# Kernel optimization log

Hardware: AMD Instinct MI355X
Metric: run time of the kernel (lower is better)

Reference implementation:

```python
import jax, jax.numpy as jnp
import numpy as np

B, N, INTER, RNN, W = 256, 128, 128, 128, 8


def _rms(x):
    # x / sqrt(mean(x^2, dim=2))
    return x / jnp.sqrt(jnp.mean(x * x, axis=2, keepdims=True))


def _sage(x, src, dst, deg, wl, bl, wr):
    # PyG SAGEConv(mean aggr, normalize=True): lin_l(mean_j x_j) + lin_r(x), then L2-normalize.
    # edge_index from torch.combinations(arange(k),2).t(): src=row0 (i<j), dst=row1;
    # batch repeat duplicates edges without node offsets -> mean unchanged, only nodes <N aggregate.
    agg = jax.ops.segment_sum(x[src], dst, num_segments=x.shape[0]) / deg[:, None]
    out = agg @ wl.T + bl + x @ wr.T
    nrm = jnp.maximum(jnp.linalg.norm(out, axis=-1, keepdims=True), 1e-12)
    return out / nrm


def setup_inputs() -> dict:
    key = jax.random.key(0)
    ks = jax.random.split(key, 32)
    g = lambda i, shape: jax.random.normal(ks[i], shape, dtype=jnp.float32) * 0.05
    return {
        'flows': jax.random.normal(ks[0], (B, N, N), dtype=jnp.float32),
        'coords_emb': jax.random.normal(ks[1], (B, N, 2 * N), dtype=jnp.float32),
        # Encoder_Coords: 4 pointwise Conv1d layers (kernel=1 == per-token Linear)
        'cw1': g(2, (INTER, 2 * N)), 'cb1': g(3, (INTER,)),
        'cw2': g(4, (2 * INTER, INTER)), 'cb2': g(5, (2 * INTER,)),
        'cw3': g(6, (RNN, 2 * INTER)), 'cb3': g(7, (RNN,)),
        'cw4': g(8, (RNN, RNN)), 'cb4': g(9, (RNN,)),
        # Encoder_Flows: 4 SAGEConv layers (lin_l with bias, lin_r no bias)
        'g1_wl': g(10, (INTER, N)), 'g1_bl': g(11, (INTER,)), 'g1_wr': g(12, (INTER, N)),
        'g2_wl': g(13, (2 * INTER, INTER)), 'g2_bl': g(14, (2 * INTER,)), 'g2_wr': g(15, (2 * INTER, INTER)),
        'g3_wl': g(16, (INTER, 2 * INTER)), 'g3_bl': g(17, (INTER,)), 'g3_wr': g(18, (INTER, 2 * INTER)),
        'g4_wl': g(19, (RNN, INTER)), 'g4_bl': g(20, (RNN,)), 'g4_wr': g(21, (RNN, INTER)),
        # Worker: per-worker Q/K projections (bias=False), stacked [W, out, in]
        'qca': g(22, (W, RNN, RNN)), 'kca': g(23, (W, RNN, RNN)),
        'qsa': g(24, (W, RNN, RNN)), 'ksa': g(25, (W, RNN, RNN)),
        # s_1s[0], s_2s[0]: Linear(N*W -> N, bias=False)
        's1w': g(26, (N, N * W)), 's2w': g(27, (N, N * W)),
    }


def reference(flows, coords_emb, cw1, cb1, cw2, cb2, cw3, cb3, cw4, cb4,
              g1_wl, g1_bl, g1_wr, g2_wl, g2_bl, g2_wr, g3_wl, g3_bl, g3_wr,
              g4_wl, g4_bl, g4_wr, qca, kca, qsa, ksa, s1w, s2w):
    # ---- rms_norm inputs (Model.action) ----
    f_in = _rms(flows)
    c_in = _rms(coords_emb)

    # ---- Encoder_Flows: SAGE stack over flattened [B*N, N] nodes ----
    x = f_in.reshape(-1, N)                      # [B*N, N]
    src, dst = jnp.triu_indices(N, k=1)          # combinations(arange(N), r=2)
    deg = jnp.maximum(
        jax.ops.segment_sum(jnp.ones_like(src, dtype=x.dtype), dst, num_segments=x.shape[0]), 1.0)
    x = _sage(x, src, dst, deg, g1_wl, g1_bl, g1_wr)
    x = _sage(x, src, dst, deg, g2_wl, g2_bl, g2_wr)
    x = _sage(x, src, dst, deg, g3_wl, g3_bl, g3_wr)
    x = _sage(x, src, dst, deg, g4_wl, g4_bl, g4_wr)
    f = _rms(jax.nn.relu(x).reshape(B, N, RNN))

    # ---- Encoder_Coords: 4 pointwise convs (no nonlinearity), attn=False ----
    c = c_in @ cw1.T + cb1
    c = c @ cw2.T + cb2
    c = c @ cw3.T + cb3
    c = c @ cw4.T + cb4
    c = _rms(c)

    # ---- Worker (dropout=0.0 -> identity) ----
    scale = jnp.sqrt(jnp.float32(RNN))
    # cross-attention branch (result discarded by Worker.forward, kept for fidelity)
    Qc = jnp.einsum('bnd,wod->bwno', f, qca)
    Kc = jnp.einsum('bmd,wod->bwmo', c, kca)
    ca = jnp.einsum('bwno,bwmo->bwnm', Qc, Kc) / scale
    ca = ca.transpose(0, 2, 3, 1).reshape(B, N, N * W) @ s1w.T  # [B,N,N], unused
    # self-attention branch (returned)
    Qs = jnp.einsum('bnd,wod->bwno', f, qsa)
    Ks = jnp.einsum('bmd,wod->bwmo', f, ksa)
    sa = jnp.einsum('bwno,bwmo->bwnm', Qs, Ks) / scale          # [B,W,N,N]
    sa = sa.transpose(0, 2, 3, 1).reshape(B, N, N * W) @ s2w.T  # [B,N,N]
    return sa
```

## Files before the change

### kernel.cpp

```cpp
#include <hip/hip_runtime.h>
#include <math.h>


typedef __attribute__((ext_vector_type(8))) short bf16x8;
typedef __attribute__((ext_vector_type(4))) float f32x4;

__device__ inline ushort f2b(float x) {
  unsigned u = __builtin_bit_cast(unsigned, x);
  unsigned r = (u + 0x7fffu + ((u >> 16) & 1u)) >> 16;
  return (ushort)r;
}
__device__ inline int ftswz(int e) { return ((e & 7) ^ ((e >> 3) & 15)) << 4; }
__device__ inline int cAddrRow(int rl) { return (rl < 8) ? rl * 512 : 8192 + (rl - 8) * 512; }

__device__ inline void ctr_signal(unsigned* c) {
  __threadfence();
  __syncthreads();
  if (threadIdx.x == 0)
    __hip_atomic_fetch_add(c, 1u, __ATOMIC_RELEASE, __HIP_MEMORY_SCOPE_AGENT);
}
__device__ inline void ctr_wait(unsigned* c, unsigned tgt) {
  if (threadIdx.x == 0) {
    while (__hip_atomic_load(c, __ATOMIC_ACQUIRE, __HIP_MEMORY_SCOPE_AGENT) < tgt)
      __builtin_amdgcn_s_sleep(8);
  }
  __syncthreads();
}

__global__ __launch_bounds__(256) void prep_all_k(
    const float* __restrict__ s2w,
    const float* __restrict__ wl1, const float* __restrict__ wl2,
    const float* __restrict__ wl3, const float* __restrict__ wl4,
    const float* __restrict__ wr1, const float* __restrict__ wr2,
    const float* __restrict__ wr3, const float* __restrict__ wr4,
    ushort* __restrict__ SBp, ushort* __restrict__ WL, ushort* __restrict__ WR,
    ushort* __restrict__ WRp, float* __restrict__ SS, unsigned* __restrict__ CTR) {
  if (blockIdx.x == 0) {
    SS[threadIdx.x] = 0.f;
    SS[threadIdx.x + 256] = 0.f;
    if (threadIdx.x < 8) CTR[threadIdx.x] = 0u;
  }
  int i = blockIdx.x * 256 + threadIdx.x;
  if (i < 131072) {
    int w = i >> 14, p = (i >> 7) & 127, m = i & 127;
    int sidx = ((((w * 2 + (p >> 6)) * 4 + ((p >> 4) & 3)) * 4 + (m >> 5)) * 64 +
                ((m >> 3) & 3) * 16 + (p & 15)) * 8 + (m & 7);
    SBp[sidx] = f2b(s2w[p * 1024 + m * 8 + w]);
    return;
  }
  i -= 131072;
  if (i < 98304) {
    float v, u;
    int base, K, col, k;
    if (i < 16384)      { v = wl1[i];         u = wr1[i];         base = 0;     K = 128; col = i >> 7;            k = i & 127; }
    else if (i < 49152) { int j = i - 16384;  v = wl2[j]; u = wr2[j]; base = 16384; K = 128; col = j >> 7;       k = j & 127; }
    else if (i < 81920) { int j = i - 49152;  v = wl3[j]; u = wr3[j]; base = 49152; K = 256; col = j >> 8;       k = j & 255; }
    else                { int j = i - 81920;  v = wl4[j]; u = wr4[j]; base = 81920; K = 128; col = j >> 7;       k = j & 127; }
    WL[i] = f2b(v);
    ushort ub = f2b(u);
    WR[i] = ub;
    int pidx = base + (((col >> 4) * (K / 32) + (k >> 5)) * 64 +
                       ((k >> 3) & 3) * 16 + (col & 15)) * 8 + (k & 7);
    WRp[pidx] = ub;
  }
}

template <int K, int N, int MODE>
__device__ void chain_dev(char* XS, char* C0T, float* sArr,
                          const float* __restrict__ flows, const ushort* __restrict__ XTsrc,
                          const float* __restrict__ SSprev,
                          const ushort* __restrict__ Wl, const ushort* __restrict__ Wr,
                          const float* __restrict__ bias,
                          ushort* __restrict__ XTdst, float* __restrict__ YTdst,
                          float* __restrict__ SScur, int cbid) {
  const int tid = threadIdx.x;
  const int lane = tid & 63, wv = tid >> 6, lr = lane & 15, lg = lane >> 4;
  const int cG = cbid * 16 + lr;
  constexpr int NH = K / 128;

  float sr[2][4];
  f32x4 acc1[2] = {{0.f,0.f,0.f,0.f},{0.f,0.f,0.f,0.f}};
  f32x4 acc2[2] = {{0.f,0.f,0.f,0.f},{0.f,0.f,0.f,0.f}};

  #pragma unroll
  for (int h = 0; h < NH; ++h) {
    __syncthreads();
    if (MODE == 0) {
      #pragma unroll
      for (int it = 0; it < 16; ++it) {
        int idx = tid + it * 256;
        int row = idx >> 5, c4 = idx & 31;
        const float4 v = *reinterpret_cast<const float4*>(flows + (size_t)row * 128 + c4 * 4);
        float ss = v.x * v.x + v.y * v.y + v.z * v.z + v.w * v.w;
        ss += __shfl_xor(ss, 16); ss += __shfl_xor(ss, 8);
        ss += __shfl_xor(ss, 4);  ss += __shfl_xor(ss, 2); ss += __shfl_xor(ss, 1);
        *reinterpret_cast<ushort*>(XS + (c4 * 4 + 0) * 272 + row * 2) = f2b(v.x);
        *reinterpret_cast<ushort*>(XS + (c4 * 4 + 1) * 272 + row * 2) = f2b(v.y);
        *reinterpret_cast<ushort*>(XS + (c4 * 4 + 2) * 272 + row * 2) = f2b(v.z);
        *reinterpret_cast<ushort*>(XS + (c4 * 4 + 3) * 272 + row * 2) = f2b(v.w);
        if ((tid & 31) == 0) sArr[row] = rsqrtf(ss * (1.0f / 128.0f));
      }
    } else {
      for (int e = tid * 8; e < 16384; e += 2048) {
        uint4 v = *reinterpret_cast<const uint4*>(XTsrc + h * 16384 + e);
        *reinterpret_cast<uint4*>(XS + (e >> 7) * 272 + (e & 127) * 2) = v;
      }
      if (h == 0 && tid < 128) sArr[tid] = 1.0f / fmaxf(sqrtf(SSprev[tid]), 1e-12f);
    }
    __syncthreads();

    #pragma unroll
    for (int mt = 0; mt < 2; ++mt) {
      int R = wv * 32 + mt * 16 + lr;
      bf16x8 a[4];
      #pragma unroll
      for (int ks = 0; ks < 4; ++ks) {
        union { ushort us[8]; bf16x8 v; } u;
        #pragma unroll
        for (int j = 0; j < 8; ++j)
          u.us[j] = *reinterpret_cast<const ushort*>(XS + (ks * 32 + lg * 8 + j) * 272 + R * 2);
        a[ks] = u.v;
      }
      if (h == 0) {
        #pragma unroll
        for (int rr = 0; rr < 4; ++rr) sr[mt][rr] = sArr[wv * 32 + mt * 16 + 4 * lg + rr];
      }
      #pragma unroll
      for (int ks = 0; ks < 4; ++ks) {
        bf16x8 bw = *reinterpret_cast<const bf16x8*>(Wl + (size_t)cG * K + h * 128 + ks * 32 + lg * 8);
        acc1[mt] = __builtin_amdgcn_mfma_f32_16x16x32_bf16(a[ks], bw, acc1[mt], 0, 0, 0);
      }
      #pragma unroll
      for (int ks = 0; ks < 4; ++ks) {
        bf16x8 bw = *reinterpret_cast<const bf16x8*>(Wr + (size_t)cG * K + h * 128 + ks * 32 + lg * 8);
        acc2[mt] = __builtin_amdgcn_mfma_f32_16x16x32_bf16(a[ks], bw, acc2[mt], 0, 0, 0);
      }
    }
  }

  bf16x8 aL[2][4];
  #pragma unroll
  for (int mt = 0; mt < 2; ++mt) {
    int rowL = wv * 32 + mt * 16 + lr;
    ushort iv = f2b(1.0f / (float)(rowL > 1 ? rowL : 1));
    #pragma unroll
    for (int ks = 0; ks < 4; ++ks)
      #pragma unroll
      for (int j = 0; j < 8; ++j) {
        int k = ks * 32 + lg * 8 + j;
        aL[mt][ks][j] = (short)((k < rowL) ? iv : 0);
      }
  }

  #pragma unroll
  for (int mt = 0; mt < 2; ++mt) {
    int m0 = wv * 32 + mt * 16 + lg * 4;
    uint2 pk;
    pk.x = (unsigned)f2b(acc1[mt][0] * sr[mt][0]) | ((unsigned)f2b(acc1[mt][1] * sr[mt][1]) << 16);
    pk.y = (unsigned)f2b(acc1[mt][2] * sr[mt][2]) | ((unsigned)f2b(acc1[mt][3] * sr[mt][3]) << 16);
    *reinterpret_cast<uint2*>(C0T + lr * 256 + ((2 * m0) ^ ((lr & 7) << 4))) = pk;
  }
  __syncthreads();

  {
    bf16x8 bc[4];
    #pragma unroll
    for (int ks = 0; ks < 4; ++ks)
      bc[ks] = *reinterpret_cast<const bf16x8*>(C0T + lr * 256 + ((ks * 64 + lg * 16) ^ ((lr & 7) << 4)));
    float bb = bias[cG];
    #pragma unroll
    for (int mt = 0; mt < 2; ++mt) {
      f32x4 cacc = {0.f, 0.f, 0.f, 0.f};
      #pragma unroll
      for (int ks = 0; ks < 4; ++ks)
        cacc = __builtin_amdgcn_mfma_f32_16x16x32_bf16(aL[mt][ks], bc[ks], cacc, 0, 0, 0);
      int m0 = wv * 32 + mt * 16 + lg * 4;
      float ssq[4];
      if (MODE < 2) {
        float y0 = acc2[mt][0] * sr[mt][0] + bb + cacc[0];
        float y1 = acc2[mt][1] * sr[mt][1] + bb + cacc[1];
        float y2 = acc2[mt][2] * sr[mt][2] + bb + cacc[2];
        float y3 = acc2[mt][3] * sr[mt][3] + bb + cacc[3];
        uint2 pk;
        pk.x = (unsigned)f2b(y0) | ((unsigned)f2b(y1) << 16);
        pk.y = (unsigned)f2b(y2) | ((unsigned)f2b(y3) << 16);
        *reinterpret_cast<uint2*>(&XTdst[(size_t)cG * 128 + m0]) = pk;
        ssq[0] = y0 * y0; ssq[1] = y1 * y1; ssq[2] = y2 * y2; ssq[3] = y3 * y3;
      } else {
        float4 vv;
        vv.x = fmaxf(acc2[mt][0] * sr[mt][0] + bb + cacc[0], 0.f);
        vv.y = fmaxf(acc2[mt][1] * sr[mt][1] + bb + cacc[1], 0.f);
        vv.z = fmaxf(acc2[mt][2] * sr[mt][2] + bb + cacc[2], 0.f);
        vv.w = fmaxf(acc2[mt][3] * sr[mt][3] + bb + cacc[3], 0.f);
        *reinterpret_cast<float4*>(&YTdst[(size_t)cG * 128 + m0]) = vv;
        ssq[0] = vv.x * vv.x; ssq[1] = vv.y * vv.y; ssq[2] = vv.z * vv.z; ssq[3] = vv.w * vv.w;
      }
      #pragma unroll
      for (int rr = 0; rr < 4; ++rr) {
        float ss = ssq[rr];
        ss += __shfl_xor(ss, 1); ss += __shfl_xor(ss, 2);
        ss += __shfl_xor(ss, 4); ss += __shfl_xor(ss, 8);
        if (lr == 0) atomicAdd(&SScur[m0 + rr], ss);
      }
    }
  }
}

__device__ inline void sage_stage(const float* __restrict__ flows, int blk,
                                  char* W, float* sArr, int wv, int lane) {
  int r2 = lane >> 5;
  int c4 = lane & 31;
  #pragma unroll
  for (int it = 0; it < 8; ++it) {
    int rl0 = it * 2;
    const float4 v = *reinterpret_cast<const float4*>(
        flows + ((size_t)blk * 64 + wv * 16 + rl0) * 128 + lane * 4);
    int rl = rl0 + r2;
    float ss = v.x * v.x + v.y * v.y + v.z * v.z + v.w * v.w;
    ss += __shfl_xor(ss, 16); ss += __shfl_xor(ss, 8);
    ss += __shfl_xor(ss, 4);  ss += __shfl_xor(ss, 2); ss += __shfl_xor(ss, 1);
    uint2 pk;
    pk.x = (unsigned)f2b(v.x) | ((unsigned)f2b(v.y) << 16);
    pk.y = (unsigned)f2b(v.z) | ((unsigned)f2b(v.w) << 16);
    *reinterpret_cast<uint2*>(W + rl * 256 + ((c4 * 8) ^ ((rl & 7) << 4))) = pk;
    if (c4 == 0) sArr[wv * 16 + rl] = rsqrtf(ss * (1.0f / 128.0f));
  }
}

template <int N, int DSTC>
__device__ inline void sage_l128(const char* src, char* dstW,
                                 const float* sP, float* sN,
                                 const ushort* __restrict__ Wrp,
                                 const float* __restrict__ bias,
                                 int wv, int lr, int lg, int l64) {
  bf16x8 a[4];
  float sr[4];
  #pragma unroll
  for (int ks = 0; ks < 4; ++ks)
    a[ks] = *reinterpret_cast<const bf16x8*>(src + lr * 256 + ((ks * 64 + lg * 16) ^ ((lr & 7) << 4)));
  #pragma unroll
  for (int rr = 0; rr < 4; ++rr) sr[rr] = sP[wv * 16 + 4 * lg + rr];
  float ssq[4] = {0.f, 0.f, 0.f, 0.f};
  #pragma unroll
  for (int nt = 0; nt < N / 16; ++nt) {
    int col = nt * 16 + lr;
    bf16x8 b[4];
    #pragma unroll
    for (int ks = 0; ks < 4; ++ks)
      b[ks] = *reinterpret_cast<const bf16x8*>(Wrp + (((size_t)nt * 4 + ks) * 64 + l64) * 8);
    f32x4 acc = {0.f, 0.f, 0.f, 0.f};
    #pragma unroll
    for (int ks = 0; ks < 4; ++ks)
      acc = __builtin_amdgcn_mfma_f32_16x16x32_bf16(a[ks], b[ks], acc, 0, 0, 0);
    float bb = bias[col];
    #pragma unroll
    for (int rr = 0; rr < 4; ++rr) {
      int rl = 4 * lg + rr;
      float y = acc[rr] * sr[rr] + bb;
      int rowbase = DSTC ? cAddrRow(rl) : rl * 256;
      *reinterpret_cast<ushort*>(dstW + rowbase + ((col * 2) ^ ((rl & 7) << 4))) = f2b(y);
      ssq[rr] += y * y;
    }
  }
  #pragma unroll
  for (int rr = 0; rr < 4; ++rr) {
    float ss = ssq[rr];
    ss += __shfl_xor(ss, 1); ss += __shfl_xor(ss, 2);
    ss += __shfl_xor(ss, 4); ss += __shfl_xor(ss, 8);
    if (lr == 0) sN[wv * 16 + 4 * lg + rr] = 1.0f / fmaxf(sqrtf(ss), 1e-12f);
  }
}

__device__ inline void sage_l3(const char* W, char* dstD,
                               const float* sP, float* sN,
                               const ushort* __restrict__ Wrp,
                               const float* __restrict__ bias,
                               int wv, int lr, int lg, int l64) {
  bf16x8 a[8];
  float sr[4];
  #pragma unroll
  for (int ks = 0; ks < 8; ++ks)
    a[ks] = *reinterpret_cast<const bf16x8*>(W + cAddrRow(lr) + ((ks * 64 + lg * 16) ^ ((lr & 7) << 4)));
  #pragma unroll
  for (int rr = 0; rr < 4; ++rr) sr[rr] = sP[wv * 16 + 4 * lg + rr];
  float ssq[4] = {0.f, 0.f, 0.f, 0.f};
  #pragma unroll
  for (int nt = 0; nt < 8; ++nt) {
    int col = nt * 16 + lr;
    f32x4 acc = {0.f, 0.f, 0.f, 0.f};
    #pragma unroll
    for (int ks = 0; ks < 8; ++ks) {
      bf16x8 b = *reinterpret_cast<const bf16x8*>(Wrp + (((size_t)nt * 8 + ks) * 64 + l64) * 8);
      acc = __builtin_amdgcn_mfma_f32_16x16x32_bf16(a[ks], b, acc, 0, 0, 0);
    }
    float bb = bias[col];
    #pragma unroll
    for (int rr = 0; rr < 4; ++rr) {
      int rl = 4 * lg + rr;
      float y = acc[rr] * sr[rr] + bb;
      *reinterpret_cast<ushort*>(dstD + rl * 256 + ((col * 2) ^ ((rl & 7) << 4))) = f2b(y);
      ssq[rr] += y * y;
    }
  }
  #pragma unroll
  for (int rr = 0; rr < 4; ++rr) {
    float ss = ssq[rr];
    ss += __shfl_xor(ss, 1); ss += __shfl_xor(ss, 2);
    ss += __shfl_xor(ss, 4); ss += __shfl_xor(ss, 8);
    if (lr == 0) sN[wv * 16 + 4 * lg + rr] = 1.0f / fmaxf(sqrtf(ss), 1e-12f);
  }
}

__device__ inline void sage_l4(const char* src, const float* sP,
                               const ushort* __restrict__ Wrp,
                               const float* __restrict__ bias,
                               int wv, int lr, int lg, int l64,
                               ushort* __restrict__ Fg, int blk) {
  bf16x8 a[4];
  float sr[4];
  #pragma unroll
  for (int ks = 0; ks < 4; ++ks)
    a[ks] = *reinterpret_cast<const bf16x8*>(src + lr * 256 + ((ks * 64 + lg * 16) ^ ((lr & 7) << 4)));
  #pragma unroll
  for (int rr = 0; rr < 4; ++rr) sr[rr] = sP[wv * 16 + 4 * lg + rr];
  float yreg[8][4];
  float ssq[4] = {0.f, 0.f, 0.f, 0.f};
  #pragma unroll
  for (int nt = 0; nt < 8; ++nt) {
    int col = nt * 16 + lr;
    bf16x8 b[4];
    #pragma unroll
    for (int ks = 0; ks < 4; ++ks)
      b[ks] = *reinterpret_cast<const bf16x8*>(Wrp + (((size_t)nt * 4 + ks) * 64 + l64) * 8);
    f32x4 acc = {0.f, 0.f, 0.f, 0.f};
    #pragma unroll
    for (int ks = 0; ks < 4; ++ks)
      acc = __builtin_amdgcn_mfma_f32_16x16x32_bf16(a[ks], b[ks], acc, 0, 0, 0);
    float bb = bias[col];
    #pragma unroll
    for (int rr = 0; rr < 4; ++rr) {
      float y = acc[rr] * sr[rr] + bb;
      yreg[nt][rr] = y;
      float v = fmaxf(y, 0.f);
      ssq[rr] += v * v;
    }
  }
  float sc[4];
  #pragma unroll
  for (int rr = 0; rr < 4; ++rr) {
    float ss = ssq[rr];
    ss += __shfl_xor(ss, 1); ss += __shfl_xor(ss, 2);
    ss += __shfl_xor(ss, 4); ss += __shfl_xor(ss, 8);
    sc[rr] = sqrtf(128.0f / fmaxf(ss, 1e-20f));
  }
  #pragma unroll
  for (int nt = 0; nt < 8; ++nt)
    #pragma unroll
    for (int rr = 0; rr < 4; ++rr) {
      int row = wv * 16 + 4 * lg + rr;
      Fg[((size_t)blk * 64 + row) * 128 + nt * 16 + lr] = f2b(fmaxf(yreg[nt][rr], 0.f) * sc[rr]);
    }
}

__global__ __launch_bounds__(256, 2) void mega3_k(
    const float* __restrict__ flows,
    const float* __restrict__ qsa, const float* __restrict__ ksa,
    const ushort* __restrict__ WL, const ushort* __restrict__ WR,
    const ushort* __restrict__ WRp,
    const float* __restrict__ bl1, const float* __restrict__ bl2,
    const float* __restrict__ bl3, const float* __restrict__ bl4,
    ushort* __restrict__ Fg, ushort* __restrict__ MBT,
    ushort* __restrict__ XT1, ushort* __restrict__ XT2, ushort* __restrict__ XT3,
    float* __restrict__ YT4, float* __restrict__ SS, unsigned* __restrict__ CTR) {
  __shared__ char L[49664];
  const int bid = blockIdx.x;
  const int tid = threadIdx.x;
  const int lane = tid & 63, wv = tid >> 6, lr = lane & 15, lg = lane >> 4;

  if (bid < 16) {
    char* XS = L;
    char* C0T = L + 34816;
    float* sArr = (float*)(L + 38912);
    int cbid = bid;
    if (cbid < 8) {
      chain_dev<128, 128, 0>(XS, C0T, sArr, flows, nullptr, nullptr,
                             WL + 0, WR + 0, bl1, XT1, nullptr, SS + 0, cbid);
      ctr_signal(&CTR[0]);
    }
    ctr_wait(&CTR[0], 8);
    chain_dev<128, 256, 1>(XS, C0T, sArr, nullptr, XT1, SS + 0,
                           WL + 16384, WR + 16384, bl2, XT2, nullptr, SS + 128, cbid);
    ctr_signal(&CTR[1]);
    ctr_wait(&CTR[1], 16);
    if (cbid < 8) {
      chain_dev<256, 128, 1>(XS, C0T, sArr, nullptr, XT2, SS + 128,
                             WL + 49152, WR + 49152, bl3, XT3, nullptr, SS + 256, cbid);
      ctr_signal(&CTR[2]);
    }
    ctr_wait(&CTR[2], 8);
    if (cbid < 8) {
      chain_dev<128, 128, 2>(XS, C0T, sArr, nullptr, XT3, SS + 256,
                             WL + 81920, WR + 81920, bl4, nullptr, YT4, SS + 384, cbid);
      ctr_signal(&CTR[3]);
    }
    ctr_wait(&CTR[3], 8);
    if (cbid < 8) {
      int t = cbid * 256 + tid;
      int r = t >> 4, cs = t & 15;
      float sc = sqrtf(128.0f / fmaxf(SS[384 + r], 1e-20f));
      ushort tmp[8];
      #pragma unroll
      for (int j = 0; j < 8; ++j) {
        int c = cs * 8 + j;
        tmp[j] = f2b(YT4[(size_t)c * 128 + r] * sc);
      }
      *reinterpret_cast<uint4*>(&Fg[(size_t)r * 128 + cs * 8]) = *reinterpret_cast<uint4*>(tmp);
    }
    return;
  }

  if (bid < 24) {
    char* QT = L;
    int w = bid - 16;
    const float* qw = qsa + (size_t)w * 16384;
    const float* kw = ksa + (size_t)w * 16384;
    for (int e = tid; e < 16384; e += 256) {
      int op = e >> 7, c = e & 127;
      int off = c * 256 + ((op * 2) ^ ((c & 7) << 4));
      *reinterpret_cast<ushort*>(QT + off) = f2b(qw[e]);
    }
    __syncthreads();
    #pragma unroll
    for (int rt = 0; rt < 2; ++rt) {
      int e = wv * 32 + rt * 16 + lr;
      bf16x8 a[4];
      #pragma unroll
      for (int ks = 0; ks < 4; ++ks) {
        union { ushort us[8]; bf16x8 v; } u;
        #pragma unroll
        for (int j = 0; j < 8; ++j)
          u.us[j] = f2b(kw[(size_t)(ks * 32 + lg * 8 + j) * 128 + e]);
        a[ks] = u.v;
      }
      #pragma unroll
      for (int ct = 0; ct < 8; ++ct) {
        int d = ct * 16 + lr;
        bf16x8 bq[4];
        #pragma unroll
        for (int ks = 0; ks < 4; ++ks)
          bq[ks] = *reinterpret_cast<const bf16x8*>(QT + d * 256 + ((ks * 64 + lg * 16) ^ ((d & 7) << 4)));
        f32x4 acc = {0.f, 0.f, 0.f, 0.f};
        #pragma unroll
        for (int ks = 0; ks < 4; ++ks)
          acc = __builtin_amdgcn_mfma_f32_16x16x32_bf16(a[ks], bq[ks], acc, 0, 0, 0);
        uint2 pk;
        pk.x = (unsigned)f2b(acc[0]) | ((unsigned)f2b(acc[1]) << 16);
        pk.y = (unsigned)f2b(acc[2]) | ((unsigned)f2b(acc[3]) << 16);
        size_t base = ((((size_t)ct * 8 + w) * 4 + wv) * 64 +
                       (size_t)(((rt * 2 + (lg >> 1)) & 3) * 16 + lr)) * 8 + (lg & 1) * 4;
        *reinterpret_cast<uint2*>(&MBT[base]) = pk;
      }
    }
    return;
  }

  char* W = L + wv * 12288;
  float* sA = (float*)(L + 49152);
  float* sB = (float*)(L + 49408);
  const int l64 = lane;
  int blk = bid - 24 + 2;
  sage_stage(flows, blk, W, sA, wv, lane);
  asm volatile("" ::: "memory");
  sage_l128<128, 0>(W, W + 4096, sA, sB, WRp + 0,     bl1, wv, lr, lg, l64);
  asm volatile("" ::: "memory");
  sage_l128<256, 1>(W + 4096, W, sB, sA, WRp + 16384, bl2, wv, lr, lg, l64);
  asm volatile("" ::: "memory");
  sage_l3(W, W + 4096, sA, sB, WRp + 49152, bl3, wv, lr, lg, l64);
  asm volatile("" ::: "memory");
  sage_l4(W + 4096, sB, WRp + 81920, bl4, wv, lr, lg, l64, Fg, blk);
}

__global__ __launch_bounds__(512, 4) void attn_fused(
    const ushort* __restrict__ F, const ushort* __restrict__ MBT,
    const ushort* __restrict__ SBp, float* __restrict__ Out) {
  __shared__ char FT[32768];
  __shared__ char RTb[32768];

  const int bq = blockIdx.x;
  const int b = bq >> 1, ph = bq & 1;
  const int tid = threadIdx.x;
  const int l = tid & 63, wv = tid >> 6;
  const int lr = l & 15, lg = l >> 4;

  const ushort* Fb = F + (size_t)b * 16384;

  #pragma unroll
  for (int it = 0; it < 4; ++it) {
    int idx = tid + it * 512;
    int m = idx >> 4, eg = idx & 15;
    uint4 v = *reinterpret_cast<const uint4*>(Fb + m * 128 + eg * 8);
    const ushort* pv = reinterpret_cast<const ushort*>(&v);
    #pragma unroll
    for (int j = 0; j < 8; ++j) {
      int e = eg * 8 + j;
      *reinterpret_cast<ushort*>(FT + e * 256 + ((m * 2) ^ ftswz(e))) = pv[j];
    }
  }

  bf16x8 fa[4];
  {
    int n = wv * 16 + lr;
    #pragma unroll
    for (int ks = 0; ks < 4; ++ks)
      fa[ks] = *reinterpret_cast<const bf16x8*>(Fb + n * 128 + ks * 32 + lg * 8);
  }
  __syncthreads();

  bf16x8 af[4];
  {
    int e = wv * 16 + lr;
    #pragma unroll
    for (int ks = 0; ks < 4; ++ks)
      af[ks] = *reinterpret_cast<const bf16x8*>(
          FT + e * 256 + ((ks * 64 + lg * 16) ^ ftswz(e)));
  }

  f32x4 zacc[4];
  #pragma unroll
  for (int pt = 0; pt < 4; ++pt) zacc[pt] = f32x4{0.f, 0.f, 0.f, 0.f};

  const int eb0 = 2 * (wv * 16 + lg * 4);

  auto Rphase = [&](int w, char* RT) {
    #pragma unroll
    for (int pt = 0; pt < 4; ++pt) {
      int p = pt * 16 + lr;
      bf16x8 bs[4];
      #pragma unroll
      for (int ks = 0; ks < 4; ++ks)
        bs[ks] = *reinterpret_cast<const bf16x8*>(
            SBp + ((((size_t)(w * 2 + ph) * 4 + pt) * 4 + ks) * 64 + l) * 8);
      f32x4 rr = {0.f, 0.f, 0.f, 0.f};
      #pragma unroll
      for (int ks = 0; ks < 4; ++ks)
        rr = __builtin_amdgcn_mfma_f32_16x16x32_bf16(af[ks], bs[ks], rr, 0, 0, 0);
      uint2 pk;
      pk.x = (unsigned)f2b(rr[0]) | ((unsigned)f2b(rr[1]) << 16);
      pk.y = (unsigned)f2b(rr[2]) | ((unsigned)f2b(rr[3]) << 16);
      *reinterpret_cast<uint2*>(RT + p * 256 + (eb0 ^ ((p & 7) << 4))) = pk;
    }
  };
  auto Zphase = [&](int w, const char* RT) {
    bf16x8 mf[4];
    #pragma unroll
    for (int ks = 0; ks < 4; ++ks)
      mf[ks] = *reinterpret_cast<const bf16x8*>(
          MBT + ((((size_t)wv * 8 + w) * 4 + ks) * 64 + l) * 8);
    #pragma unroll
    for (int pt = 0; pt < 4; ++pt) {
      int p = pt * 16 + lr;
      bf16x8 bg[4];
      #pragma unroll
      for (int ks = 0; ks < 4; ++ks)
        bg[ks] = *reinterpret_cast<const bf16x8*>(
            RT + p * 256 + ((ks * 64 + lg * 16) ^ ((p & 7) << 4)));
      #pragma unroll
      for (int ks = 0; ks < 4; ++ks)
        zacc[pt] = __builtin_amdgcn_mfma_f32_16x16x32_bf16(mf[ks], bg[ks], zacc[pt], 0, 0, 0);
    }
  };

  Rphase(0, RTb);
  __syncthreads();
  #pragma unroll
  for (int w = 0; w < 7; ++w) {
    Zphase(w, RTb + (w & 1) * 16384);
    Rphase(w + 1, RTb + ((w + 1) & 1) * 16384);
    __syncthreads();
  }
  Zphase(7, RTb + 16384);
  #pragma unroll
  for (int pt = 0; pt < 4; ++pt) {
    int p = pt * 16 + lr;
    uint2 pk;
    pk.x = (unsigned)f2b(zacc[pt][0]) | ((unsigned)f2b(zacc[pt][1]) << 16);
    pk.y = (unsigned)f2b(zacc[pt][2]) | ((unsigned)f2b(zacc[pt][3]) << 16);
    *reinterpret_cast<uint2*>(RTb + p * 256 + (eb0 ^ ((p & 7) << 4))) = pk;
  }
  __syncthreads();

  const float inv_scale = 0.08838834764831845f;
  float* ob = Out + (size_t)b * 16384 + ph * 64;
  #pragma unroll
  for (int pt = 0; pt < 4; ++pt) {
    int p = pt * 16 + lr;
    bf16x8 bz[4];
    #pragma unroll
    for (int ks = 0; ks < 4; ++ks)
      bz[ks] = *reinterpret_cast<const bf16x8*>(
          RTb + p * 256 + ((ks * 64 + lg * 16) ^ ((p & 7) << 4)));
    f32x4 oa = {0.f, 0.f, 0.f, 0.f};
    #pragma unroll
    for (int ks = 0; ks < 4; ++ks)
      oa = __builtin_amdgcn_mfma_f32_16x16x32_bf16(fa[ks], bz[ks], oa, 0, 0, 0);
    int n0 = wv * 16 + lg * 4;
    #pragma unroll
    for (int r = 0; r < 4; ++r)
      ob[(size_t)(n0 + r) * 128 + p] = oa[r] * inv_scale;
  }
}

extern "C" void kernel_launch(void* const* d_in, const int* in_sizes, int n_in,
                              void* d_out, int out_size, void* d_ws, size_t ws_size,
                              hipStream_t stream) {
  const float* flows = (const float*)d_in[0];
  const float* g1_wl = (const float*)d_in[10];
  const float* g1_bl = (const float*)d_in[11];
  const float* g1_wr = (const float*)d_in[12];
  const float* g2_wl = (const float*)d_in[13];
  const float* g2_bl = (const float*)d_in[14];
  const float* g2_wr = (const float*)d_in[15];
  const float* g3_wl = (const float*)d_in[16];
  const float* g3_bl = (const float*)d_in[17];
  const float* g3_wr = (const float*)d_in[18];
  const float* g4_wl = (const float*)d_in[19];
  const float* g4_bl = (const float*)d_in[20];
  const float* g4_wr = (const float*)d_in[21];
  const float* qsa   = (const float*)d_in[24];
  const float* ksa   = (const float*)d_in[25];
  const float* s2w   = (const float*)d_in[27];
  float* out = (float*)d_out;
  char* wsb  = (char*)d_ws;

  ushort* FB16 = (ushort*)(wsb);
  ushort* SBp  = (ushort*)(wsb + 8388608);
  ushort* WL   = (ushort*)(wsb + 8650752);
  ushort* WR   = (ushort*)(wsb + 8847360);
  ushort* MBT  = (ushort*)(wsb + 9043968);
  ushort* XT1  = (ushort*)(wsb + 9306112);
  ushort* XT2  = (ushort*)(wsb + 9338880);
  ushort* XT3  = (ushort*)(wsb + 9404416);
  float*  YT4  = (float*)(wsb + 9437184);
  float*  SS   = (float*)(wsb + 9502720);
  ushort* WRp  = (ushort*)(wsb + 9504768);
  unsigned* CTR = (unsigned*)(wsb + 9701376);

  prep_all_k<<<896, 256, 0, stream>>>(s2w,
                                      g1_wl, g2_wl, g3_wl, g4_wl,
                                      g1_wr, g2_wr, g3_wr, g4_wr,
                                      SBp, WL, WR, WRp, SS, CTR);
  mega3_k<<<534, 256, 0, stream>>>(flows, qsa, ksa, WL, WR, WRp,
                                   g1_bl, g2_bl, g3_bl, g4_bl,
                                   FB16, MBT, XT1, XT2, XT3, YT4, SS, CTR);
  attn_fused<<<512, 512, 0, stream>>>(FB16, MBT, SBp, out);
}
```

Before: 86.70 us.

## Run batch-0 SAGE chain in one block, dropping inter-block counters and atomics

The first batch's four SAGE layers were previously split across 16 blocks that synchronized through global atomic counters and accumulated row norms with global atomicAdd. This is replaced by a single block that computes every output column block itself, keeps row sums of squares in shared memory, and reads A operands directly from row-major global activations. The goal is to remove spin-wait barriers, fences and atomic traffic and to launch fewer blocks. In exchange, one block now does all the chain's work serially, which may lengthen the critical path if that block finishes after the rest of the grid.

```diff
diff --git a/kernel.cpp b/kernel.cpp
--- a/kernel.cpp
+++ b/kernel.cpp
@@ -12,20 +12,6 @@
 }
 __device__ inline int ftswz(int e) { return ((e & 7) ^ ((e >> 3) & 15)) << 4; }
 __device__ inline int cAddrRow(int rl) { return (rl < 8) ? rl * 512 : 8192 + (rl - 8) * 512; }
-
-__device__ inline void ctr_signal(unsigned* c) {
-  __threadfence();
-  __syncthreads();
-  if (threadIdx.x == 0)
-    __hip_atomic_fetch_add(c, 1u, __ATOMIC_RELEASE, __HIP_MEMORY_SCOPE_AGENT);
-}
-__device__ inline void ctr_wait(unsigned* c, unsigned tgt) {
-  if (threadIdx.x == 0) {
-    while (__hip_atomic_load(c, __ATOMIC_ACQUIRE, __HIP_MEMORY_SCOPE_AGENT) < tgt)
-      __builtin_amdgcn_s_sleep(8);
-  }
-  __syncthreads();
-}
 
 __global__ __launch_bounds__(256) void prep_all_k(
     const float* __restrict__ s2w,
@@ -34,12 +20,7 @@
     const float* __restrict__ wr1, const float* __restrict__ wr2,
     const float* __restrict__ wr3, const float* __restrict__ wr4,
     ushort* __restrict__ SBp, ushort* __restrict__ WL, ushort* __restrict__ WR,
-    ushort* __restrict__ WRp, float* __restrict__ SS, unsigned* __restrict__ CTR) {
-  if (blockIdx.x == 0) {
-    SS[threadIdx.x] = 0.f;
-    SS[threadIdx.x + 256] = 0.f;
-    if (threadIdx.x < 8) CTR[threadIdx.x] = 0u;
-  }
+    ushort* __restrict__ WRp) {
   int i = blockIdx.x * 256 + threadIdx.x;
   if (i < 131072) {
     int w = i >> 14, p = (i >> 7) & 127, m = i & 127;
@@ -66,77 +47,56 @@
 }
 
 template <int K, int N, int MODE>
-__device__ void chain_dev(char* XS, char* C0T, float* sArr,
-                          const float* __restrict__ flows, const ushort* __restrict__ XTsrc,
-                          const float* __restrict__ SSprev,
-                          const ushort* __restrict__ Wl, const ushort* __restrict__ Wr,
-                          const float* __restrict__ bias,
-                          ushort* __restrict__ XTdst, float* __restrict__ YTdst,
-                          float* __restrict__ SScur, int cbid) {
+__device__ void chainS_dev(char* C0T, float* sArr, float* sSS,
+                           const float* __restrict__ flows,
+                           const ushort* __restrict__ XRsrc,
+                           const ushort* __restrict__ Wl, const ushort* __restrict__ Wr,
+                           const float* __restrict__ bias,
+                           ushort* __restrict__ XRdst, float* __restrict__ YTdst) {
   const int tid = threadIdx.x;
   const int lane = tid & 63, wv = tid >> 6, lr = lane & 15, lg = lane >> 4;
-  const int cG = cbid * 16 + lr;
-  constexpr int NH = K / 128;
+  constexpr int NF = K / 32;
+  constexpr int NCB = N / 16;
+
+  __syncthreads();
+
+  bf16x8 a[2][NF];
+  #pragma unroll
+  for (int mt = 0; mt < 2; ++mt) {
+    int R = wv * 32 + mt * 16 + lr;
+    if (MODE == 0) {
+      float ssq = 0.f;
+      #pragma unroll
+      for (int ks = 0; ks < NF; ++ks) {
+        const float4 v0 = *reinterpret_cast<const float4*>(flows + (size_t)R * K + ks * 32 + lg * 8);
+        const float4 v1 = *reinterpret_cast<const float4*>(flows + (size_t)R * K + ks * 32 + lg * 8 + 4);
+        ssq += v0.x * v0.x + v0.y * v0.y + v0.z * v0.z + v0.w * v0.w;
+        ssq += v1.x * v1.x + v1.y * v1.y + v1.z * v1.z + v1.w * v1.w;
+        union { ushort us[8]; bf16x8 v; } u;
+        u.us[0] = f2b(v0.x); u.us[1] = f2b(v0.y); u.us[2] = f2b(v0.z); u.us[3] = f2b(v0.w);
+        u.us[4] = f2b(v1.x); u.us[5] = f2b(v1.y); u.us[6] = f2b(v1.z); u.us[7] = f2b(v1.w);
+        a[mt][ks] = u.v;
+      }
+      ssq += __shfl_xor(ssq, 16);
+      ssq += __shfl_xor(ssq, 32);
+      if (lg == 0) sArr[R] = rsqrtf(ssq * (1.0f / 128.0f));
+    } else {
+      #pragma unroll
+      for (int ks = 0; ks < NF; ++ks)
+        a[mt][ks] = *reinterpret_cast<const bf16x8*>(XRsrc + (size_t)R * K + ks * 32 + lg * 8);
+    }
+  }
+  if (MODE != 0) {
+    if (tid < 128) sArr[tid] = 1.0f / fmaxf(sqrtf(sSS[tid]), 1e-12f);
+  }
+  __syncthreads();
 
   float sr[2][4];
-  f32x4 acc1[2] = {{0.f,0.f,0.f,0.f},{0.f,0.f,0.f,0.f}};
-  f32x4 acc2[2] = {{0.f,0.f,0.f,0.f},{0.f,0.f,0.f,0.f}};
-
-  #pragma unroll
-  for (int h = 0; h < NH; ++h) {
-    __syncthreads();
-    if (MODE == 0) {
-      #pragma unroll
-      for (int it = 0; it < 16; ++it) {
-        int idx = tid + it * 256;
-        int row = idx >> 5, c4 = idx & 31;
-        const float4 v = *reinterpret_cast<const float4*>(flows + (size_t)row * 128 + c4 * 4);
-        float ss = v.x * v.x + v.y * v.y + v.z * v.z + v.w * v.w;
-        ss += __shfl_xor(ss, 16); ss += __shfl_xor(ss, 8);
-        ss += __shfl_xor(ss, 4);  ss += __shfl_xor(ss, 2); ss += __shfl_xor(ss, 1);
-        *reinterpret_cast<ushort*>(XS + (c4 * 4 + 0) * 272 + row * 2) = f2b(v.x);
-        *reinterpret_cast<ushort*>(XS + (c4 * 4 + 1) * 272 + row * 2) = f2b(v.y);
-        *reinterpret_cast<ushort*>(XS + (c4 * 4 + 2) * 272 + row * 2) = f2b(v.z);
-        *reinterpret_cast<ushort*>(XS + (c4 * 4 + 3) * 272 + row * 2) = f2b(v.w);
-        if ((tid & 31) == 0) sArr[row] = rsqrtf(ss * (1.0f / 128.0f));
-      }
-    } else {
-      for (int e = tid * 8; e < 16384; e += 2048) {
-        uint4 v = *reinterpret_cast<const uint4*>(XTsrc + h * 16384 + e);
-        *reinterpret_cast<uint4*>(XS + (e >> 7) * 272 + (e & 127) * 2) = v;
-      }
-      if (h == 0 && tid < 128) sArr[tid] = 1.0f / fmaxf(sqrtf(SSprev[tid]), 1e-12f);
-    }
-    __syncthreads();
-
-    #pragma unroll
-    for (int mt = 0; mt < 2; ++mt) {
-      int R = wv * 32 + mt * 16 + lr;
-      bf16x8 a[4];
-      #pragma unroll
-      for (int ks = 0; ks < 4; ++ks) {
-        union { ushort us[8]; bf16x8 v; } u;
-        #pragma unroll
-        for (int j = 0; j < 8; ++j)
-          u.us[j] = *reinterpret_cast<const ushort*>(XS + (ks * 32 + lg * 8 + j) * 272 + R * 2);
-        a[ks] = u.v;
-      }
-      if (h == 0) {
-        #pragma unroll
-        for (int rr = 0; rr < 4; ++rr) sr[mt][rr] = sArr[wv * 32 + mt * 16 + 4 * lg + rr];
-      }
-      #pragma unroll
-      for (int ks = 0; ks < 4; ++ks) {
-        bf16x8 bw = *reinterpret_cast<const bf16x8*>(Wl + (size_t)cG * K + h * 128 + ks * 32 + lg * 8);
-        acc1[mt] = __builtin_amdgcn_mfma_f32_16x16x32_bf16(a[ks], bw, acc1[mt], 0, 0, 0);
-      }
-      #pragma unroll
-      for (int ks = 0; ks < 4; ++ks) {
-        bf16x8 bw = *reinterpret_cast<const bf16x8*>(Wr + (size_t)cG * K + h * 128 + ks * 32 + lg * 8);
-        acc2[mt] = __builtin_amdgcn_mfma_f32_16x16x32_bf16(a[ks], bw, acc2[mt], 0, 0, 0);
-      }
-    }
-  }
+  #pragma unroll
+  for (int mt = 0; mt < 2; ++mt)
+    #pragma unroll
+    for (int rr = 0; rr < 4; ++rr)
+      sr[mt][rr] = sArr[wv * 32 + mt * 16 + 4 * lg + rr];
 
   bf16x8 aL[2][4];
   #pragma unroll
@@ -152,58 +112,87 @@
       }
   }
 
-  #pragma unroll
-  for (int mt = 0; mt < 2; ++mt) {
-    int m0 = wv * 32 + mt * 16 + lg * 4;
-    uint2 pk;
-    pk.x = (unsigned)f2b(acc1[mt][0] * sr[mt][0]) | ((unsigned)f2b(acc1[mt][1] * sr[mt][1]) << 16);
-    pk.y = (unsigned)f2b(acc1[mt][2] * sr[mt][2]) | ((unsigned)f2b(acc1[mt][3] * sr[mt][3]) << 16);
-    *reinterpret_cast<uint2*>(C0T + lr * 256 + ((2 * m0) ^ ((lr & 7) << 4))) = pk;
-  }
-  __syncthreads();
-
-  {
-    bf16x8 bc[4];
-    #pragma unroll
-    for (int ks = 0; ks < 4; ++ks)
-      bc[ks] = *reinterpret_cast<const bf16x8*>(C0T + lr * 256 + ((ks * 64 + lg * 16) ^ ((lr & 7) << 4)));
-    float bb = bias[cG];
-    #pragma unroll
-    for (int mt = 0; mt < 2; ++mt) {
-      f32x4 cacc = {0.f, 0.f, 0.f, 0.f};
+  float ssqo[2][4] = {{0.f, 0.f, 0.f, 0.f}, {0.f, 0.f, 0.f, 0.f}};
+
+  constexpr int NCH = (NCB + 7) / 8;
+  #pragma unroll
+  for (int ch = 0; ch < NCH; ++ch) {
+    #pragma unroll
+    for (int cb8 = 0; cb8 < 8; ++cb8) {
+      int cb = ch * 8 + cb8;
+      int cG = cb * 16 + lr;
+      f32x4 acc[2] = {{0.f, 0.f, 0.f, 0.f}, {0.f, 0.f, 0.f, 0.f}};
+      #pragma unroll
+      for (int ks = 0; ks < NF; ++ks) {
+        bf16x8 bw = *reinterpret_cast<const bf16x8*>(Wl + (size_t)cG * K + ks * 32 + lg * 8);
+        acc[0] = __builtin_amdgcn_mfma_f32_16x16x32_bf16(a[0][ks], bw, acc[0], 0, 0, 0);
+        acc[1] = __builtin_amdgcn_mfma_f32_16x16x32_bf16(a[1][ks], bw, acc[1], 0, 0, 0);
+      }
+      #pragma unroll
+      for (int mt = 0; mt < 2; ++mt) {
+        int m0 = wv * 32 + mt * 16 + lg * 4;
+        uint2 pk;
+        pk.x = (unsigned)f2b(acc[mt][0] * sr[mt][0]) | ((unsigned)f2b(acc[mt][1] * sr[mt][1]) << 16);
+        pk.y = (unsigned)f2b(acc[mt][2] * sr[mt][2]) | ((unsigned)f2b(acc[mt][3] * sr[mt][3]) << 16);
+        *reinterpret_cast<uint2*>(C0T + cb8 * 4096 + lr * 256 + ((2 * m0) ^ ((lr & 7) << 4))) = pk;
+      }
+    }
+    __syncthreads();
+    #pragma unroll
+    for (int cb8 = 0; cb8 < 8; ++cb8) {
+      int cb = ch * 8 + cb8;
+      int cG = cb * 16 + lr;
+      f32x4 acc[2] = {{0.f, 0.f, 0.f, 0.f}, {0.f, 0.f, 0.f, 0.f}};
+      #pragma unroll
+      for (int ks = 0; ks < NF; ++ks) {
+        bf16x8 bw = *reinterpret_cast<const bf16x8*>(Wr + (size_t)cG * K + ks * 32 + lg * 8);
+        acc[0] = __builtin_amdgcn_mfma_f32_16x16x32_bf16(a[0][ks], bw, acc[0], 0, 0, 0);
+        acc[1] = __builtin_amdgcn_mfma_f32_16x16x32_bf16(a[1][ks], bw, acc[1], 0, 0, 0);
+      }
+      bf16x8 bc[4];
       #pragma unroll
       for (int ks = 0; ks < 4; ++ks)
-        cacc = __builtin_amdgcn_mfma_f32_16x16x32_bf16(aL[mt][ks], bc[ks], cacc, 0, 0, 0);
-      int m0 = wv * 32 + mt * 16 + lg * 4;
-      float ssq[4];
-      if (MODE < 2) {
-        float y0 = acc2[mt][0] * sr[mt][0] + bb + cacc[0];
-        float y1 = acc2[mt][1] * sr[mt][1] + bb + cacc[1];
-        float y2 = acc2[mt][2] * sr[mt][2] + bb + cacc[2];
-        float y3 = acc2[mt][3] * sr[mt][3] + bb + cacc[3];
-        uint2 pk;
-        pk.x = (unsigned)f2b(y0) | ((unsigned)f2b(y1) << 16);
-        pk.y = (unsigned)f2b(y2) | ((unsigned)f2b(y3) << 16);
-        *reinterpret_cast<uint2*>(&XTdst[(size_t)cG * 128 + m0]) = pk;
-        ssq[0] = y0 * y0; ssq[1] = y1 * y1; ssq[2] = y2 * y2; ssq[3] = y3 * y3;
-      } else {
-        float4 vv;
-        vv.x = fmaxf(acc2[mt][0] * sr[mt][0] + bb + cacc[0], 0.f);
-        vv.y = fmaxf(acc2[mt][1] * sr[mt][1] + bb + cacc[1], 0.f);
-        vv.z = fmaxf(acc2[mt][2] * sr[mt][2] + bb + cacc[2], 0.f);
-        vv.w = fmaxf(acc2[mt][3] * sr[mt][3] + bb + cacc[3], 0.f);
-        *reinterpret_cast<float4*>(&YTdst[(size_t)cG * 128 + m0]) = vv;
-        ssq[0] = vv.x * vv.x; ssq[1] = vv.y * vv.y; ssq[2] = vv.z * vv.z; ssq[3] = vv.w * vv.w;
-      }
-      #pragma unroll
-      for (int rr = 0; rr < 4; ++rr) {
-        float ss = ssq[rr];
-        ss += __shfl_xor(ss, 1); ss += __shfl_xor(ss, 2);
-        ss += __shfl_xor(ss, 4); ss += __shfl_xor(ss, 8);
-        if (lr == 0) atomicAdd(&SScur[m0 + rr], ss);
-      }
-    }
-  }
+        bc[ks] = *reinterpret_cast<const bf16x8*>(
+            C0T + cb8 * 4096 + lr * 256 + ((ks * 64 + lg * 16) ^ ((lr & 7) << 4)));
+      float bb = bias[cG];
+      #pragma unroll
+      for (int mt = 0; mt < 2; ++mt) {
+        f32x4 cacc = {0.f, 0.f, 0.f, 0.f};
+        #pragma unroll
+        for (int ks = 0; ks < 4; ++ks)
+          cacc = __builtin_amdgcn_mfma_f32_16x16x32_bf16(aL[mt][ks], bc[ks], cacc, 0, 0, 0);
+        int m0 = wv * 32 + mt * 16 + lg * 4;
+        if (MODE < 2) {
+          #pragma unroll
+          for (int rr = 0; rr < 4; ++rr) {
+            float y = acc[mt][rr] * sr[mt][rr] + bb + cacc[rr];
+            XRdst[(size_t)(m0 + rr) * N + cG] = f2b(y);
+            ssqo[mt][rr] += y * y;
+          }
+        } else {
+          float4 vv;
+          vv.x = fmaxf(acc[mt][0] * sr[mt][0] + bb + cacc[0], 0.f);
+          vv.y = fmaxf(acc[mt][1] * sr[mt][1] + bb + cacc[1], 0.f);
+          vv.z = fmaxf(acc[mt][2] * sr[mt][2] + bb + cacc[2], 0.f);
+          vv.w = fmaxf(acc[mt][3] * sr[mt][3] + bb + cacc[3], 0.f);
+          *reinterpret_cast<float4*>(&YTdst[(size_t)cG * 128 + m0]) = vv;
+          ssqo[mt][0] += vv.x * vv.x; ssqo[mt][1] += vv.y * vv.y;
+          ssqo[mt][2] += vv.z * vv.z; ssqo[mt][3] += vv.w * vv.w;
+        }
+      }
+    }
+    __syncthreads();
+  }
+
+  #pragma unroll
+  for (int mt = 0; mt < 2; ++mt)
+    #pragma unroll
+    for (int rr = 0; rr < 4; ++rr) {
+      float ss = ssqo[mt][rr];
+      ss += __shfl_xor(ss, 1); ss += __shfl_xor(ss, 2);
+      ss += __shfl_xor(ss, 4); ss += __shfl_xor(ss, 8);
+      if (lr == 0) sSS[wv * 32 + mt * 16 + 4 * lg + rr] = ss;
+    }
 }
 
 __device__ inline void sage_stage(const float* __restrict__ flows, int blk,
@@ -362,7 +351,7 @@
     }
 }
 
-__global__ __launch_bounds__(256, 2) void mega3_k(
+__global__ __launch_bounds__(256, 2) void mega4_k(
     const float* __restrict__ flows,
     const float* __restrict__ qsa, const float* __restrict__ ksa,
     const ushort* __restrict__ WL, const ushort* __restrict__ WR,
@@ -371,43 +360,26 @@
     const float* __restrict__ bl3, const float* __restrict__ bl4,
     ushort* __restrict__ Fg, ushort* __restrict__ MBT,
     ushort* __restrict__ XT1, ushort* __restrict__ XT2, ushort* __restrict__ XT3,
-    float* __restrict__ YT4, float* __restrict__ SS, unsigned* __restrict__ CTR) {
+    float* __restrict__ YT4) {
   __shared__ char L[49664];
   const int bid = blockIdx.x;
   const int tid = threadIdx.x;
   const int lane = tid & 63, wv = tid >> 6, lr = lane & 15, lg = lane >> 4;
 
-  if (bid < 16) {
-    char* XS = L;
-    char* C0T = L + 34816;
-    float* sArr = (float*)(L + 38912);
-    int cbid = bid;
-    if (cbid < 8) {
-      chain_dev<128, 128, 0>(XS, C0T, sArr, flows, nullptr, nullptr,
-                             WL + 0, WR + 0, bl1, XT1, nullptr, SS + 0, cbid);
-      ctr_signal(&CTR[0]);
-    }
-    ctr_wait(&CTR[0], 8);
-    chain_dev<128, 256, 1>(XS, C0T, sArr, nullptr, XT1, SS + 0,
-                           WL + 16384, WR + 16384, bl2, XT2, nullptr, SS + 128, cbid);
-    ctr_signal(&CTR[1]);
-    ctr_wait(&CTR[1], 16);
-    if (cbid < 8) {
-      chain_dev<256, 128, 1>(XS, C0T, sArr, nullptr, XT2, SS + 128,
-                             WL + 49152, WR + 49152, bl3, XT3, nullptr, SS + 256, cbid);
-      ctr_signal(&CTR[2]);
-    }
-    ctr_wait(&CTR[2], 8);
-    if (cbid < 8) {
-      chain_dev<128, 128, 2>(XS, C0T, sArr, nullptr, XT3, SS + 256,
-                             WL + 81920, WR + 81920, bl4, nullptr, YT4, SS + 384, cbid);
-      ctr_signal(&CTR[3]);
-    }
-    ctr_wait(&CTR[3], 8);
-    if (cbid < 8) {
-      int t = cbid * 256 + tid;
+  if (bid == 0) {
+    char* C0T = L;
+    float* sArr = (float*)(L + 32768);
+    float* sSS = (float*)(L + 33280);
+    chainS_dev<128, 128, 0>(C0T, sArr, sSS, flows, nullptr, WL + 0, WR + 0, bl1, XT1, nullptr);
+    chainS_dev<128, 256, 1>(C0T, sArr, sSS, nullptr, XT1, WL + 16384, WR + 16384, bl2, XT2, nullptr);
+    chainS_dev<256, 128, 1>(C0T, sArr, sSS, nullptr, XT2, WL + 49152, WR + 49152, bl3, XT3, nullptr);
+    chainS_dev<128, 128, 2>(C0T, sArr, sSS, nullptr, XT3, WL + 81920, WR + 81920, bl4, nullptr, YT4);
+    __syncthreads();
+    #pragma unroll
+    for (int i = 0; i < 8; ++i) {
+      int t = i * 256 + tid;
       int r = t >> 4, cs = t & 15;
-      float sc = sqrtf(128.0f / fmaxf(SS[384 + r], 1e-20f));
+      float sc = sqrtf(128.0f / fmaxf(sSS[r], 1e-20f));
       ushort tmp[8];
       #pragma unroll
       for (int j = 0; j < 8; ++j) {
@@ -419,9 +391,9 @@
     return;
   }
 
-  if (bid < 24) {
+  if (bid < 9) {
     char* QT = L;
-    int w = bid - 16;
+    int w = bid - 1;
     const float* qw = qsa + (size_t)w * 16384;
     const float* kw = ksa + (size_t)w * 16384;
     for (int e = tid; e < 16384; e += 256) {
@@ -468,7 +440,7 @@
   float* sA = (float*)(L + 49152);
   float* sB = (float*)(L + 49408);
   const int l64 = lane;
-  int blk = bid - 24 + 2;
+  int blk = bid - 9 + 2;
   sage_stage(flows, blk, W, sA, wv, lane);
   asm volatile("" ::: "memory");
   sage_l128<128, 0>(W, W + 4096, sA, sB, WRp + 0,     bl1, wv, lr, lg, l64);
@@ -641,16 +613,14 @@
   ushort* XT2  = (ushort*)(wsb + 9338880);
   ushort* XT3  = (ushort*)(wsb + 9404416);
   float*  YT4  = (float*)(wsb + 9437184);
-  float*  SS   = (float*)(wsb + 9502720);
   ushort* WRp  = (ushort*)(wsb + 9504768);
-  unsigned* CTR = (unsigned*)(wsb + 9701376);
 
   prep_all_k<<<896, 256, 0, stream>>>(s2w,
                                       g1_wl, g2_wl, g3_wl, g4_wl,
                                       g1_wr, g2_wr, g3_wr, g4_wr,
-                                      SBp, WL, WR, WRp, SS, CTR);
-  mega3_k<<<534, 256, 0, stream>>>(flows, qsa, ksa, WL, WR, WRp,
+                                      SBp, WL, WR, WRp);
+  mega4_k<<<519, 256, 0, stream>>>(flows, qsa, ksa, WL, WR, WRp,
                                    g1_bl, g2_bl, g3_bl, g4_bl,
-                                   FB16, MBT, XT1, XT2, XT3, YT4, SS, CTR);
+                                   FB16, MBT, XT1, XT2, XT3, YT4);
   attn_fused<<<512, 512, 0, stream>>>(FB16, MBT, SBp, out);
 }
```

After: 142.3 us. +64.1%, slower.
